# Performance work log

Measured on AMD Instinct MI355X. Metric: run time of the kernel, lower is better.

Reference implementation:

```python
import jax, jax.numpy as jnp
import numpy as np

D_MODEL = 256
NUM_HEADS = 8
D_HEAD = D_MODEL // NUM_HEADS


def setup_inputs() -> dict:
    key = jax.random.key(0)
    k1, k2, k3, k4, k5, k6 = jax.random.split(key, 6)
    B, L, C, H, W = 2, 2048, D_MODEL, 4, 4
    query = jax.random.normal(k1, (B, L, C, H, W), dtype=jnp.float32)
    key_t = jax.random.normal(k2, (B, L, C, H, W), dtype=jnp.float32)
    value = jax.random.normal(k3, (B, L, C, H, W), dtype=jnp.float32)
    # 1x1 conv weights (out_channels, in_channels), no bias
    s = 1.0 / np.sqrt(C)
    Wq = jax.random.uniform(k4, (C, C), jnp.float32, -s, s)
    Wk = jax.random.uniform(k5, (C, C), jnp.float32, -s, s)
    Wv = jax.random.uniform(k6, (C, C), jnp.float32, -s, s)
    return {"query": query, "key": key_t, "value": value, "Wq": Wq, "Wk": Wk, "Wv": Wv}


def _split_heads(x, B, L, H, W):
    # (B, L, C, H, W) -> (num_heads*B, L, d_head, H, W), head-major like torch permute(2,0,1,3,4,5)
    x = x.reshape(B, L, NUM_HEADS, D_HEAD, H, W)
    x = jnp.transpose(x, (2, 0, 1, 3, 4, 5))  # (nh, B, L, d_head, H, W)
    return x.reshape(NUM_HEADS * B, L, D_HEAD, H, W)


def reference(query, key, value, Wq, Wk, Wv):
    B, L, C, H, W = value.shape
    # 1x1 conv == channel matmul: (B,L,C,H,W) x (O,C) -> (B,L,O,H,W)
    q = jnp.einsum('blchw,oc->blohw', query, Wq)
    k = jnp.einsum('blchw,oc->blohw', key, Wk)
    v = jnp.einsum('blchw,oc->blohw', value, Wv)
    q = _split_heads(q, B, L, H, W)
    k = _split_heads(k, B, L, H, W)
    v = _split_heads(v, B, L, H, W)
    scale = 1.0 / np.sqrt(D_HEAD).astype(np.float32)
    score = jnp.einsum('bidhw,bjdhw->bij', q, k) * scale  # (nh*B, L, L)
    attn = jax.nn.softmax(score, axis=-1)
    context = jnp.einsum('bij,bjdhw->bidhw', attn, v)  # (nh*B, L, d_head, H, W)
    context = context.reshape(NUM_HEADS, B, L, D_HEAD, H, W)
    context = jnp.transpose(context, (1, 2, 0, 3, 4, 5)).reshape(B, L, C, H, W)
    return context, attn
```

## Files before the change

### kernel.cpp

```cpp
#include <hip/hip_runtime.h>


typedef short s16x8 __attribute__((ext_vector_type(8)));
typedef float f32x4 __attribute__((ext_vector_type(4)));

__device__ __forceinline__ unsigned short f2bf(float f) {
  union { float f; unsigned int u; } v; v.f = f;
  return (unsigned short)((v.u + 0x7FFFu + ((v.u >> 16) & 1u)) >> 16);
}
__device__ __forceinline__ float bf2f(unsigned short h) {
  union { unsigned int u; float f; } v; v.u = ((unsigned int)h) << 16;
  return v.f;
}

__device__ __forceinline__ void async_copy16(const unsigned short* g, unsigned short* l) {
  __builtin_amdgcn_global_load_lds((const __attribute__((address_space(1))) void*)g,
                                   (__attribute__((address_space(3))) void*)l, 16, 0, 0);
}

__global__ void __launch_bounds__(256) prep_x_kernel(const float* __restrict__ src,
                                                     unsigned short* __restrict__ dst) {
  __shared__ float ld[256 * 17];
  const int bl = blockIdx.x;
  const int t = threadIdx.x;
  const float* s = src + (size_t)bl * 4096;
#pragma unroll
  for (int i = 0; i < 4; ++i) {
    int flat = i * 1024 + t * 4;
    float4 v = *(const float4*)(s + flat);
    int c = flat >> 4, hw = flat & 15;
    float* p = &ld[c * 17 + hw];
    p[0] = v.x; p[1] = v.y; p[2] = v.z; p[3] = v.w;
  }
  __syncthreads();
  unsigned short* d = dst + (size_t)bl * 4096;
#pragma unroll
  for (int hw = 0; hw < 16; ++hw)
    d[hw * 256 + t] = f2bf(ld[t * 17 + hw]);
}

__global__ void __launch_bounds__(256) prep_xv_kernel(const float* __restrict__ src,
                                                      unsigned short* __restrict__ dst) {
  __shared__ float ld[256 * 17];
  const int bl = blockIdx.x;
  const int b = bl >> 11, l = bl & 2047;
  const int t = threadIdx.x;
  const float* s = src + (size_t)bl * 4096;
#pragma unroll
  for (int i = 0; i < 4; ++i) {
    int flat = i * 1024 + t * 4;
    float4 v = *(const float4*)(s + flat);
    int c = flat >> 4, hw = flat & 15;
    float* p = &ld[c * 17 + hw];
    p[0] = v.x; p[1] = v.y; p[2] = v.z; p[3] = v.w;
  }
  __syncthreads();
#pragma unroll
  for (int hw = 0; hw < 16; ++hw)
    dst[((size_t)(b * 16 + hw) * 2048 + l) * 256 + t] = f2bf(ld[t * 17 + hw]);
}

__global__ void __launch_bounds__(256) prep_w_kernel(const float* __restrict__ a,
                                                     const float* __restrict__ b,
                                                     const float* __restrict__ c,
                                                     unsigned short* __restrict__ dst) {
  int i = blockIdx.x * 256 + threadIdx.x;
  const float* s = (i < 65536) ? a : ((i < 131072) ? b : c);
  dst[i] = f2bf(s[i & 65535]);
}

__device__ __forceinline__ void gemm_core_async(const unsigned short* __restrict__ Ag, int ldA,
                                                const unsigned short* __restrict__ Bg, int ldB,
                                                int K, unsigned short* As, unsigned short* Bs,
                                                f32x4 acc[4][4]) {
  const int tid = threadIdx.x;
  const int lane = tid & 63;
  const int w = tid >> 6;
  const int wr = (w >> 1) * 64, wc = (w & 1) * 64;
  const int r = lane >> 2, kk = (lane & 3) * 8;
  for (int k0 = 0; k0 < K; k0 += 32) {
#pragma unroll
    for (int i = 0; i < 2; ++i) {
      const int row0 = w * 32 + i * 16;
      async_copy16(Ag + (size_t)(row0 + r) * ldA + k0 + kk, As + row0 * 32);
      async_copy16(Bg + (size_t)(row0 + r) * ldB + k0 + kk, Bs + row0 * 32);
    }
    __syncthreads();
    s16x8 af[4], bfv[4];
#pragma unroll
    for (int m = 0; m < 4; ++m)
      af[m] = *(const s16x8*)(As + (wr + m * 16 + (lane & 15)) * 32 + (lane >> 4) * 8);
#pragma unroll
    for (int n = 0; n < 4; ++n)
      bfv[n] = *(const s16x8*)(Bs + (wc + n * 16 + (lane & 15)) * 32 + (lane >> 4) * 8);
#pragma unroll
    for (int m = 0; m < 4; ++m)
#pragma unroll
      for (int n = 0; n < 4; ++n)
        acc[m][n] = __builtin_amdgcn_mfma_f32_16x16x32_bf16(af[m], bfv[n], acc[m][n], 0, 0, 0);
    __syncthreads();
  }
}

#define ACC_INIT(acc)                         \
  {                                           \
    const f32x4 z_ = {0.f, 0.f, 0.f, 0.f};    \
    _Pragma("unroll")                         \
    for (int m_ = 0; m_ < 4; ++m_)            \
      _Pragma("unroll")                       \
      for (int n_ = 0; n_ < 4; ++n_) acc[m_][n_] = z_; \
  }

__global__ void __launch_bounds__(256) gemm_proj_kernel(const unsigned short* __restrict__ X,
                                                        const unsigned short* __restrict__ W,
                                                        unsigned short* __restrict__ out) {
  __shared__ unsigned short As[4096], Bs[4096];
  f32x4 acc[4][4];
  ACC_INIT(acc);
  gemm_core_async(X + (size_t)blockIdx.x * 128 * 256, 256,
                  W + (size_t)blockIdx.y * 128 * 256, 256, 256, As, Bs, acc);
  const int tid = threadIdx.x, lane = tid & 63, w = tid >> 6;
  const int wr = (w >> 1) * 64, wc = (w & 1) * 64;
  const int R0 = blockIdx.x * 128 + wr + ((lane >> 4) << 2);
  const int C0 = blockIdx.y * 128 + wc + (lane & 15);
#pragma unroll
  for (int m = 0; m < 4; ++m)
#pragma unroll
    for (int n = 0; n < 4; ++n)
#pragma unroll
      for (int r = 0; r < 4; ++r) {
        int R = R0 + m * 16 + r;
        int o = C0 + n * 16;
        int bl = R >> 4, hw = R & 15;
        int b = bl >> 11, l = bl & 2047;
        int head = o >> 5, d = o & 31;
        out[((size_t)(head * 2 + b) * 2048 + l) * 512 + d * 16 + hw] = f2bf(acc[m][n][r]);
      }
}

__global__ void __launch_bounds__(256) gemm_proj_vt_kernel(const unsigned short* __restrict__ W,
                                                           const unsigned short* __restrict__ X2,
                                                           unsigned short* __restrict__ vt) {
  __shared__ unsigned short As[4096], Bs[4096];
  f32x4 acc[4][4];
  ACC_INIT(acc);
  gemm_core_async(W + (size_t)blockIdx.x * 128 * 256, 256,
                  X2 + (size_t)blockIdx.y * 128 * 256, 256, 256, As, Bs, acc);
  const int tid = threadIdx.x, lane = tid & 63, w = tid >> 6;
  const int wr = (w >> 1) * 64, wc = (w & 1) * 64;
  const int R0 = blockIdx.x * 128 + wr + ((lane >> 4) << 2);
  const int C0 = blockIdx.y * 128 + wc + (lane & 15);
#pragma unroll
  for (int m = 0; m < 4; ++m)
#pragma unroll
    for (int n = 0; n < 4; ++n)
#pragma unroll
      for (int r = 0; r < 4; ++r) {
        int o = R0 + m * 16 + r;
        int p = C0 + n * 16;
        int head = o >> 5, d = o & 31;
        int b = p >> 15, hw = (p >> 11) & 15, l = p & 2047;
        vt[((size_t)((head * 2 + b) * 512) + d * 16 + hw) * 2048 + l] = f2bf(acc[m][n][r]);
      }
}

template <int FUSED>
__global__ void __launch_bounds__(256) gemm_score_kernel(const unsigned short* __restrict__ q,
                                                         const unsigned short* __restrict__ k,
                                                         float* __restrict__ attn,
                                                         unsigned short* __restrict__ pbf,
                                                         float* __restrict__ partial) {
  __shared__ unsigned short As[4096], Bs[4096];
  f32x4 acc[4][4];
  ACC_INIT(acc);
  const int bh = blockIdx.z;
  gemm_core_async(q + ((size_t)bh * 2048 + blockIdx.x * 128) * 512, 512,
                  k + ((size_t)bh * 2048 + blockIdx.y * 128) * 512, 512, 512, As, Bs, acc);
  const int tid = threadIdx.x, lane = tid & 63, w = tid >> 6;
  const int wr = (w >> 1) * 64, wc = (w & 1) * 64;
  const float scale = 0.17677669529663687f;
  const int R0 = blockIdx.x * 128 + wr + ((lane >> 4) << 2);
  const int C0 = blockIdx.y * 128 + wc + (lane & 15);
  if (!FUSED) {
    float* O = attn + (size_t)bh * 4194304;
#pragma unroll
    for (int m = 0; m < 4; ++m)
#pragma unroll
      for (int n = 0; n < 4; ++n)
#pragma unroll
        for (int r = 0; r < 4; ++r)
          O[(size_t)(R0 + m * 16 + r) * 2048 + (C0 + n * 16)] = acc[m][n][r] * scale;
  } else {
#pragma unroll
    for (int m = 0; m < 4; ++m)
#pragma unroll
      for (int n = 0; n < 4; ++n)
#pragma unroll
        for (int r = 0; r < 4; ++r)
          acc[m][n][r] = __expf(acc[m][n][r] * scale);
    unsigned short* P = pbf + (size_t)bh * 4194304;
#pragma unroll
    for (int m = 0; m < 4; ++m)
#pragma unroll
      for (int n = 0; n < 4; ++n)
#pragma unroll
        for (int r = 0; r < 4; ++r)
          P[(size_t)(R0 + m * 16 + r) * 2048 + (C0 + n * 16)] = f2bf(acc[m][n][r]);
    const int chunk = blockIdx.y * 2 + (w & 1);
#pragma unroll
    for (int m = 0; m < 4; ++m)
#pragma unroll
      for (int r = 0; r < 4; ++r) {
        float s = (acc[m][0][r] + acc[m][1][r]) + (acc[m][2][r] + acc[m][3][r]);
        s += __shfl_xor(s, 1); s += __shfl_xor(s, 2);
        s += __shfl_xor(s, 4); s += __shfl_xor(s, 8);
        if ((lane & 15) == 0) {
          int rloc = wr + ((lane >> 4) << 2) + m * 16 + r;
          partial[((size_t)bh * 2048 + blockIdx.x * 128 + rloc) * 32 + chunk] = s;
        }
      }
  }
}

__global__ void __launch_bounds__(256) norm_kernel(const unsigned short* __restrict__ pbf,
                                                   const float* __restrict__ partial,
                                                   float* __restrict__ attn,
                                                   float* __restrict__ inv_buf) {
  __shared__ float sh;
  const int row = blockIdx.x;
  const int t = threadIdx.x;
  if (t < 32) {
    float v = partial[(size_t)row * 32 + t];
    v += __shfl_xor(v, 1); v += __shfl_xor(v, 2);
    v += __shfl_xor(v, 4); v += __shfl_xor(v, 8); v += __shfl_xor(v, 16);
    if (t == 0) sh = v;
  }
  __syncthreads();
  const float inv = 1.0f / sh;
  if (t == 0) inv_buf[row] = inv;
  s16x8 h = *(const s16x8*)(pbf + (size_t)row * 2048 + t * 8);
  float o[8];
#pragma unroll
  for (int i = 0; i < 8; ++i) o[i] = bf2f((unsigned short)h[i]) * inv;
  float* p = attn + (size_t)row * 2048 + t * 8;
  *(float4*)(p)     = *(float4*)&o[0];
  *(float4*)(p + 4) = *(float4*)&o[4];
}

__global__ void __launch_bounds__(256) softmax_kernel(float* __restrict__ attn) {
  __shared__ float red[4];
  float* p = attn + (size_t)blockIdx.x * 2048;
  const int t = threadIdx.x;
  float4 v0 = *(const float4*)(p + t * 8);
  float4 v1 = *(const float4*)(p + t * 8 + 4);
  float mx = fmaxf(fmaxf(fmaxf(v0.x, v0.y), fmaxf(v0.z, v0.w)),
                   fmaxf(fmaxf(v1.x, v1.y), fmaxf(v1.z, v1.w)));
#pragma unroll
  for (int off = 32; off; off >>= 1) mx = fmaxf(mx, __shfl_xor(mx, off));
  if ((t & 63) == 0) red[t >> 6] = mx;
  __syncthreads();
  mx = fmaxf(fmaxf(red[0], red[1]), fmaxf(red[2], red[3]));
  __syncthreads();
  float e[8];
  e[0] = __expf(v0.x - mx); e[1] = __expf(v0.y - mx);
  e[2] = __expf(v0.z - mx); e[3] = __expf(v0.w - mx);
  e[4] = __expf(v1.x - mx); e[5] = __expf(v1.y - mx);
  e[6] = __expf(v1.z - mx); e[7] = __expf(v1.w - mx);
  float s = ((e[0] + e[1]) + (e[2] + e[3])) + ((e[4] + e[5]) + (e[6] + e[7]));
#pragma unroll
  for (int off = 32; off; off >>= 1) s += __shfl_xor(s, off);
  if ((t & 63) == 0) red[t >> 6] = s;
  __syncthreads();
  s = red[0] + red[1] + red[2] + red[3];
  const float inv = 1.0f / s;
  float4 o0 = {e[0] * inv, e[1] * inv, e[2] * inv, e[3] * inv};
  float4 o1 = {e[4] * inv, e[5] * inv, e[6] * inv, e[7] * inv};
  *(float4*)(p + t * 8) = o0;
  *(float4*)(p + t * 8 + 4) = o1;
}

__global__ void __launch_bounds__(256) transpose_v_kernel(const unsigned short* __restrict__ vs,
                                                          unsigned short* __restrict__ vt) {
  __shared__ unsigned short tile[64][65];
  const int bh = blockIdx.z;
  const int j0 = blockIdx.x * 64, d0 = blockIdx.y * 64;
  const unsigned short* src = vs + (size_t)bh * 2048 * 512;
  unsigned short* dst = vt + (size_t)bh * 512 * 2048;
  const int t = threadIdx.x;
#pragma unroll
  for (int i = 0; i < 16; ++i) {
    int e = t * 16 + i;
    int r = e >> 6, c = e & 63;
    tile[r][c] = src[(size_t)(j0 + r) * 512 + d0 + c];
  }
  __syncthreads();
#pragma unroll
  for (int i = 0; i < 16; ++i) {
    int e = t * 16 + i;
    int r = e >> 6, c = e & 63;
    dst[(size_t)(d0 + r) * 2048 + j0 + c] = tile[c][r];
  }
}

__device__ __forceinline__ void ctx_epilogue(f32x4 acc[4][4], float* __restrict__ outc,
                                             const float* __restrict__ inv_buf,
                                             int bh, int bx, int by) {
  const int tid = threadIdx.x, lane = tid & 63, w = tid >> 6;
  const int wr = (w >> 1) * 64, wc = (w & 1) * 64;
  const int b = bh & 1, head = bh >> 1;
  const int R0 = bx * 128 + wr + ((lane >> 4) << 2);
  const int C0 = by * 128 + wc + (lane & 15);
#pragma unroll
  for (int m = 0; m < 4; ++m)
#pragma unroll
    for (int r2 = 0; r2 < 4; ++r2) {
      int R = R0 + m * 16 + r2;
      float sc = inv_buf ? inv_buf[(size_t)bh * 2048 + R] : 1.0f;
#pragma unroll
      for (int n = 0; n < 4; ++n) {
        int dd = C0 + n * 16;
        int d = dd >> 4, hw = dd & 15;
        outc[((size_t)(b * 2048 + R) * 256 + head * 32 + d) * 16 + hw] = acc[m][n][r2] * sc;
      }
    }
}

__global__ void __launch_bounds__(256) gemm_ctx_bf16_kernel(const unsigned short* __restrict__ pbf,
                                                            const unsigned short* __restrict__ vt,
                                                            const float* __restrict__ inv_buf,
                                                            float* __restrict__ outc) {
  __shared__ unsigned short As[4096], Bs[4096];
  f32x4 acc[4][4];
  ACC_INIT(acc);
  const int bh = blockIdx.z;
  gemm_core_async(pbf + (size_t)bh * 4194304 + (size_t)blockIdx.x * 128 * 2048, 2048,
                  vt + (size_t)bh * 1048576 + (size_t)blockIdx.y * 128 * 2048, 2048,
                  2048, As, Bs, acc);
  ctx_epilogue(acc, outc, inv_buf, bh, blockIdx.x, blockIdx.y);
}

__global__ void __launch_bounds__(256) gemm_ctx_f32_kernel(const float* __restrict__ attn,
                                                           const unsigned short* __restrict__ vt,
                                                           float* __restrict__ outc) {
  __shared__ unsigned short As[4096], Bs[4096];
  f32x4 acc[4][4];
  ACC_INIT(acc);
  const int tid = threadIdx.x, lane = tid & 63, w = tid >> 6;
  const int wr = (w >> 1) * 64, wc = (w & 1) * 64;
  const int bh = blockIdx.z;
  const float* Ag = attn + (size_t)bh * 4194304 + (size_t)blockIdx.x * 128 * 2048;
  const unsigned short* Bg = vt + (size_t)bh * 1048576 + (size_t)blockIdx.y * 128 * 2048;
  const int r = lane >> 2, kk = (lane & 3) * 8;
  const int arow = tid >> 1, acol = (tid & 1) * 16;
  for (int k0 = 0; k0 < 2048; k0 += 32) {
#pragma unroll
    for (int i = 0; i < 2; ++i) {
      const int row0 = w * 32 + i * 16;
      async_copy16(Bg + (size_t)(row0 + r) * 2048 + k0 + kk, Bs + row0 * 32);
    }
    {
      const float* sp = Ag + (size_t)arow * 2048 + k0 + acol;
      float4 f0 = *(const float4*)(sp);
      float4 f1 = *(const float4*)(sp + 4);
      float4 f2 = *(const float4*)(sp + 8);
      float4 f3 = *(const float4*)(sp + 12);
      s16x8 h0, h1;
      h0[0] = (short)f2bf(f0.x); h0[1] = (short)f2bf(f0.y);
      h0[2] = (short)f2bf(f0.z); h0[3] = (short)f2bf(f0.w);
      h0[4] = (short)f2bf(f1.x); h0[5] = (short)f2bf(f1.y);
      h0[6] = (short)f2bf(f1.z); h0[7] = (short)f2bf(f1.w);
      h1[0] = (short)f2bf(f2.x); h1[1] = (short)f2bf(f2.y);
      h1[2] = (short)f2bf(f2.z); h1[3] = (short)f2bf(f2.w);
      h1[4] = (short)f2bf(f3.x); h1[5] = (short)f2bf(f3.y);
      h1[6] = (short)f2bf(f3.z); h1[7] = (short)f2bf(f3.w);
      *(s16x8*)(As + arow * 32 + acol) = h0;
      *(s16x8*)(As + arow * 32 + acol + 8) = h1;
    }
    __syncthreads();
    s16x8 af[4], bfv[4];
#pragma unroll
    for (int m = 0; m < 4; ++m)
      af[m] = *(const s16x8*)(As + (wr + m * 16 + (lane & 15)) * 32 + (lane >> 4) * 8);
#pragma unroll
    for (int n = 0; n < 4; ++n)
      bfv[n] = *(const s16x8*)(Bs + (wc + n * 16 + (lane & 15)) * 32 + (lane >> 4) * 8);
#pragma unroll
    for (int m = 0; m < 4; ++m)
#pragma unroll
      for (int n = 0; n < 4; ++n)
        acc[m][n] = __builtin_amdgcn_mfma_f32_16x16x32_bf16(af[m], bfv[n], acc[m][n], 0, 0, 0);
    __syncthreads();
  }
  ctx_epilogue(acc, outc, nullptr, bh, blockIdx.x, blockIdx.y);
}

extern "C" void kernel_launch(void* const* d_in, const int* in_sizes, int n_in,
                              void* d_out, int out_size, void* d_ws, size_t ws_size,
                              hipStream_t stream) {
  const float* query = (const float*)d_in[0];
  const float* key   = (const float*)d_in[1];
  const float* value = (const float*)d_in[2];
  const float* Wq    = (const float*)d_in[3];
  const float* Wk    = (const float*)d_in[4];
  const float* Wv    = (const float*)d_in[5];

  float* out_ctx  = (float*)d_out;
  float* out_attn = (float*)d_out + 16777216;

  unsigned short* X    = (unsigned short*)d_ws;
  unsigned short* q_s  = X + 16777216;
  unsigned short* k_s  = q_s + 16777216;
  unsigned short* v_t  = k_s + 16777216;
  unsigned short* Wbf  = v_t + 16777216;
  unsigned short* P_bf = Wbf + 196608;
  float* partial = (float*)(P_bf + 67108864);
  float* inv_buf = partial + 1048576;

  const bool fused = ws_size >= (size_t)273154048;

  prep_w_kernel<<<768, 256, 0, stream>>>(Wq, Wk, Wv, Wbf);

  prep_x_kernel<<<4096, 256, 0, stream>>>(query, X);
  gemm_proj_kernel<<<dim3(512, 2), 256, 0, stream>>>(X, Wbf, q_s);

  prep_x_kernel<<<4096, 256, 0, stream>>>(key, X);
  gemm_proj_kernel<<<dim3(512, 2), 256, 0, stream>>>(X, Wbf + 65536, k_s);

  if (fused) {
    prep_xv_kernel<<<4096, 256, 0, stream>>>(value, X);
    gemm_proj_vt_kernel<<<dim3(2, 512), 256, 0, stream>>>(Wbf + 131072, X, v_t);
    gemm_score_kernel<1><<<dim3(16, 16, 16), 256, 0, stream>>>(q_s, k_s, nullptr, P_bf, partial);
    norm_kernel<<<32768, 256, 0, stream>>>(P_bf, partial, out_attn, inv_buf);
    gemm_ctx_bf16_kernel<<<dim3(16, 4, 16), 256, 0, stream>>>(P_bf, v_t, inv_buf, out_ctx);
  } else {
    prep_x_kernel<<<4096, 256, 0, stream>>>(value, X);
    gemm_proj_kernel<<<dim3(512, 2), 256, 0, stream>>>(X, Wbf + 131072, v_t);
    gemm_score_kernel<0><<<dim3(16, 16, 16), 256, 0, stream>>>(q_s, k_s, out_attn, nullptr, nullptr);
    softmax_kernel<<<32768, 256, 0, stream>>>(out_attn);
    transpose_v_kernel<<<dim3(32, 8, 16), 256, 0, stream>>>(v_t, X);
    gemm_ctx_f32_kernel<<<dim3(16, 4, 16), 256, 0, stream>>>(out_attn, X, out_ctx);
  }
}
```

Before: 478.5 us.

## Fuse attn normalization into ctx GEMM and batch Q/K/V prep and projections

Merges the three input prep launches into one kernel and the Q/K projections into one batched launch, staging Xq/Xk in the P_bf buffer before it is overwritten. The separate norm pass that re-read bf16 probabilities and wrote fp32 attn is replaced by a tiny inv-sum kernel. The y==0 blocks of the context GEMM now write normalized attn straight from the LDS tiles they already load. This removes one full re-read of the probability matrix and several launches, but leaves the attn store work on only a quarter of the ctx blocks, which may unbalance that kernel.

```diff
diff --git a/kernel.cpp b/kernel.cpp
--- a/kernel.cpp
+++ b/kernel.cpp
@@ -16,6 +16,39 @@
 __device__ __forceinline__ void async_copy16(const unsigned short* g, unsigned short* l) {
   __builtin_amdgcn_global_load_lds((const __attribute__((address_space(1))) void*)g,
                                    (__attribute__((address_space(3))) void*)l, 16, 0, 0);
+}
+
+__global__ void __launch_bounds__(256) prep_all_kernel(const float* __restrict__ qs,
+                                                       const float* __restrict__ ks,
+                                                       const float* __restrict__ vs,
+                                                       unsigned short* __restrict__ Xq,
+                                                       unsigned short* __restrict__ Xk,
+                                                       unsigned short* __restrict__ X2) {
+  __shared__ float ld[256 * 17];
+  const int bl = blockIdx.x;
+  const int z = blockIdx.y;
+  const int t = threadIdx.x;
+  const float* s = (z == 0 ? qs : (z == 1 ? ks : vs)) + (size_t)bl * 4096;
+#pragma unroll
+  for (int i = 0; i < 4; ++i) {
+    int flat = i * 1024 + t * 4;
+    float4 v = *(const float4*)(s + flat);
+    int c = flat >> 4, hw = flat & 15;
+    float* p = &ld[c * 17 + hw];
+    p[0] = v.x; p[1] = v.y; p[2] = v.z; p[3] = v.w;
+  }
+  __syncthreads();
+  if (z < 2) {
+    unsigned short* d = (z == 0 ? Xq : Xk) + (size_t)bl * 4096;
+#pragma unroll
+    for (int hw = 0; hw < 16; ++hw)
+      d[hw * 256 + t] = f2bf(ld[t * 17 + hw]);
+  } else {
+    const int b = bl >> 11, l = bl & 2047;
+#pragma unroll
+    for (int hw = 0; hw < 16; ++hw)
+      X2[((size_t)(b * 16 + hw) * 2048 + l) * 256 + t] = f2bf(ld[t * 17 + hw]);
+  }
 }
 
 __global__ void __launch_bounds__(256) prep_x_kernel(const float* __restrict__ src,
@@ -37,27 +70,6 @@
 #pragma unroll
   for (int hw = 0; hw < 16; ++hw)
     d[hw * 256 + t] = f2bf(ld[t * 17 + hw]);
-}
-
-__global__ void __launch_bounds__(256) prep_xv_kernel(const float* __restrict__ src,
-                                                      unsigned short* __restrict__ dst) {
-  __shared__ float ld[256 * 17];
-  const int bl = blockIdx.x;
-  const int b = bl >> 11, l = bl & 2047;
-  const int t = threadIdx.x;
-  const float* s = src + (size_t)bl * 4096;
-#pragma unroll
-  for (int i = 0; i < 4; ++i) {
-    int flat = i * 1024 + t * 4;
-    float4 v = *(const float4*)(s + flat);
-    int c = flat >> 4, hw = flat & 15;
-    float* p = &ld[c * 17 + hw];
-    p[0] = v.x; p[1] = v.y; p[2] = v.z; p[3] = v.w;
-  }
-  __syncthreads();
-#pragma unroll
-  for (int hw = 0; hw < 16; ++hw)
-    dst[((size_t)(b * 16 + hw) * 2048 + l) * 256 + t] = f2bf(ld[t * 17 + hw]);
 }
 
 __global__ void __launch_bounds__(256) prep_w_kernel(const float* __restrict__ a,
@@ -110,6 +122,39 @@
       _Pragma("unroll")                       \
       for (int n_ = 0; n_ < 4; ++n_) acc[m_][n_] = z_; \
   }
+
+__global__ void __launch_bounds__(256) gemm_proj_qk_kernel(const unsigned short* __restrict__ Xq,
+                                                           const unsigned short* __restrict__ Xk,
+                                                           const unsigned short* __restrict__ Wbf,
+                                                           unsigned short* __restrict__ q_s,
+                                                           unsigned short* __restrict__ k_s) {
+  __shared__ unsigned short As[4096], Bs[4096];
+  f32x4 acc[4][4];
+  ACC_INIT(acc);
+  const int z = blockIdx.z;
+  const unsigned short* X = z ? Xk : Xq;
+  const unsigned short* W = Wbf + z * 65536;
+  unsigned short* out = z ? k_s : q_s;
+  gemm_core_async(X + (size_t)blockIdx.x * 128 * 256, 256,
+                  W + (size_t)blockIdx.y * 128 * 256, 256, 256, As, Bs, acc);
+  const int tid = threadIdx.x, lane = tid & 63, w = tid >> 6;
+  const int wr = (w >> 1) * 64, wc = (w & 1) * 64;
+  const int R0 = blockIdx.x * 128 + wr + ((lane >> 4) << 2);
+  const int C0 = blockIdx.y * 128 + wc + (lane & 15);
+#pragma unroll
+  for (int m = 0; m < 4; ++m)
+#pragma unroll
+    for (int n = 0; n < 4; ++n)
+#pragma unroll
+      for (int r = 0; r < 4; ++r) {
+        int R = R0 + m * 16 + r;
+        int o = C0 + n * 16;
+        int bl = R >> 4, hw = R & 15;
+        int b = bl >> 11, l = bl & 2047;
+        int head = o >> 5, d = o & 31;
+        out[((size_t)(head * 2 + b) * 2048 + l) * 512 + d * 16 + hw] = f2bf(acc[m][n][r]);
+      }
+}
 
 __global__ void __launch_bounds__(256) gemm_proj_kernel(const unsigned short* __restrict__ X,
                                                         const unsigned short* __restrict__ W,
@@ -222,29 +267,100 @@
   }
 }
 
-__global__ void __launch_bounds__(256) norm_kernel(const unsigned short* __restrict__ pbf,
-                                                   const float* __restrict__ partial,
-                                                   float* __restrict__ attn,
-                                                   float* __restrict__ inv_buf) {
-  __shared__ float sh;
-  const int row = blockIdx.x;
+__global__ void __launch_bounds__(256) inv_kernel(const float* __restrict__ partial,
+                                                  float* __restrict__ inv_buf) {
   const int t = threadIdx.x;
-  if (t < 32) {
-    float v = partial[(size_t)row * 32 + t];
-    v += __shfl_xor(v, 1); v += __shfl_xor(v, 2);
-    v += __shfl_xor(v, 4); v += __shfl_xor(v, 8); v += __shfl_xor(v, 16);
-    if (t == 0) sh = v;
-  }
-  __syncthreads();
-  const float inv = 1.0f / sh;
-  if (t == 0) inv_buf[row] = inv;
-  s16x8 h = *(const s16x8*)(pbf + (size_t)row * 2048 + t * 8);
-  float o[8];
-#pragma unroll
-  for (int i = 0; i < 8; ++i) o[i] = bf2f((unsigned short)h[i]) * inv;
-  float* p = attn + (size_t)row * 2048 + t * 8;
-  *(float4*)(p)     = *(float4*)&o[0];
-  *(float4*)(p + 4) = *(float4*)&o[4];
+  const int row = blockIdx.x * 64 + (t >> 2);
+  const int q4 = t & 3;
+  const float4* p = (const float4*)(partial + (size_t)row * 32 + q4 * 8);
+  float4 a = p[0], b = p[1];
+  float s = ((a.x + a.y) + (a.z + a.w)) + ((b.x + b.y) + (b.z + b.w));
+  s += __shfl_xor(s, 1); s += __shfl_xor(s, 2);
+  if (q4 == 0) inv_buf[row] = 1.0f / s;
+}
+
+__device__ __forceinline__ void ctx_epilogue(f32x4 acc[4][4], float* __restrict__ outc,
+                                             const float* __restrict__ inv_buf,
+                                             int bh, int bx, int by) {
+  const int tid = threadIdx.x, lane = tid & 63, w = tid >> 6;
+  const int wr = (w >> 1) * 64, wc = (w & 1) * 64;
+  const int b = bh & 1, head = bh >> 1;
+  const int R0 = bx * 128 + wr + ((lane >> 4) << 2);
+  const int C0 = by * 128 + wc + (lane & 15);
+#pragma unroll
+  for (int m = 0; m < 4; ++m)
+#pragma unroll
+    for (int r2 = 0; r2 < 4; ++r2) {
+      int R = R0 + m * 16 + r2;
+      float sc = inv_buf ? inv_buf[(size_t)bh * 2048 + R] : 1.0f;
+#pragma unroll
+      for (int n = 0; n < 4; ++n) {
+        int dd = C0 + n * 16;
+        int d = dd >> 4, hw = dd & 15;
+        outc[((size_t)(b * 2048 + R) * 256 + head * 32 + d) * 16 + hw] = acc[m][n][r2] * sc;
+      }
+    }
+}
+
+__global__ void __launch_bounds__(256) gemm_ctx_fused_kernel(const unsigned short* __restrict__ pbf,
+                                                             const unsigned short* __restrict__ vt,
+                                                             const float* __restrict__ inv_buf,
+                                                             float* __restrict__ attn,
+                                                             float* __restrict__ outc) {
+  __shared__ unsigned short As[4096], Bs[4096];
+  f32x4 acc[4][4];
+  ACC_INIT(acc);
+  const int tid = threadIdx.x, lane = tid & 63, w = tid >> 6;
+  const int wr = (w >> 1) * 64, wc = (w & 1) * 64;
+  const int bh = blockIdx.z;
+  const unsigned short* Ag = pbf + (size_t)bh * 4194304 + (size_t)blockIdx.x * 128 * 2048;
+  const unsigned short* Bg = vt + (size_t)bh * 1048576 + (size_t)blockIdx.y * 128 * 2048;
+  const int r = lane >> 2, kk = (lane & 3) * 8;
+  const bool emit = (blockIdx.y == 0);
+  const int erow = tid >> 1, ecol = (tid & 1) * 16;
+  float einv = 0.f;
+  float* eattn = nullptr;
+  if (emit) {
+    einv = inv_buf[(size_t)bh * 2048 + blockIdx.x * 128 + erow];
+    eattn = attn + (size_t)bh * 4194304 + (size_t)(blockIdx.x * 128 + erow) * 2048 + ecol;
+  }
+  for (int k0 = 0; k0 < 2048; k0 += 32) {
+#pragma unroll
+    for (int i = 0; i < 2; ++i) {
+      const int row0 = w * 32 + i * 16;
+      async_copy16(Ag + (size_t)(row0 + r) * 2048 + k0 + kk, As + row0 * 32);
+      async_copy16(Bg + (size_t)(row0 + r) * 2048 + k0 + kk, Bs + row0 * 32);
+    }
+    __syncthreads();
+    if (emit) {
+      s16x8 h0 = *(const s16x8*)(As + erow * 32 + ecol);
+      s16x8 h1 = *(const s16x8*)(As + erow * 32 + ecol + 8);
+      float o[16];
+#pragma unroll
+      for (int i = 0; i < 8; ++i) o[i] = bf2f((unsigned short)h0[i]) * einv;
+#pragma unroll
+      for (int i = 0; i < 8; ++i) o[8 + i] = bf2f((unsigned short)h1[i]) * einv;
+      float* ep = eattn + k0;
+      *(float4*)(ep)      = *(float4*)&o[0];
+      *(float4*)(ep + 4)  = *(float4*)&o[4];
+      *(float4*)(ep + 8)  = *(float4*)&o[8];
+      *(float4*)(ep + 12) = *(float4*)&o[12];
+    }
+    s16x8 af[4], bfv[4];
+#pragma unroll
+    for (int m = 0; m < 4; ++m)
+      af[m] = *(const s16x8*)(As + (wr + m * 16 + (lane & 15)) * 32 + (lane >> 4) * 8);
+#pragma unroll
+    for (int n = 0; n < 4; ++n)
+      bfv[n] = *(const s16x8*)(Bs + (wc + n * 16 + (lane & 15)) * 32 + (lane >> 4) * 8);
+#pragma unroll
+    for (int m = 0; m < 4; ++m)
+#pragma unroll
+      for (int n = 0; n < 4; ++n)
+        acc[m][n] = __builtin_amdgcn_mfma_f32_16x16x32_bf16(af[m], bfv[n], acc[m][n], 0, 0, 0);
+    __syncthreads();
+  }
+  ctx_epilogue(acc, outc, inv_buf, bh, blockIdx.x, blockIdx.y);
 }
 
 __global__ void __launch_bounds__(256) softmax_kernel(float* __restrict__ attn) {
@@ -300,43 +416,6 @@
     int r = e >> 6, c = e & 63;
     dst[(size_t)(d0 + r) * 2048 + j0 + c] = tile[c][r];
   }
-}
-
-__device__ __forceinline__ void ctx_epilogue(f32x4 acc[4][4], float* __restrict__ outc,
-                                             const float* __restrict__ inv_buf,
-                                             int bh, int bx, int by) {
-  const int tid = threadIdx.x, lane = tid & 63, w = tid >> 6;
-  const int wr = (w >> 1) * 64, wc = (w & 1) * 64;
-  const int b = bh & 1, head = bh >> 1;
-  const int R0 = bx * 128 + wr + ((lane >> 4) << 2);
-  const int C0 = by * 128 + wc + (lane & 15);
-#pragma unroll
-  for (int m = 0; m < 4; ++m)
-#pragma unroll
-    for (int r2 = 0; r2 < 4; ++r2) {
-      int R = R0 + m * 16 + r2;
-      float sc = inv_buf ? inv_buf[(size_t)bh * 2048 + R] : 1.0f;
-#pragma unroll
-      for (int n = 0; n < 4; ++n) {
-        int dd = C0 + n * 16;
-        int d = dd >> 4, hw = dd & 15;
-        outc[((size_t)(b * 2048 + R) * 256 + head * 32 + d) * 16 + hw] = acc[m][n][r2] * sc;
-      }
-    }
-}
-
-__global__ void __launch_bounds__(256) gemm_ctx_bf16_kernel(const unsigned short* __restrict__ pbf,
-                                                            const unsigned short* __restrict__ vt,
-                                                            const float* __restrict__ inv_buf,
-                                                            float* __restrict__ outc) {
-  __shared__ unsigned short As[4096], Bs[4096];
-  f32x4 acc[4][4];
-  ACC_INIT(acc);
-  const int bh = blockIdx.z;
-  gemm_core_async(pbf + (size_t)bh * 4194304 + (size_t)blockIdx.x * 128 * 2048, 2048,
-                  vt + (size_t)bh * 1048576 + (size_t)blockIdx.y * 128 * 2048, 2048,
-                  2048, As, Bs, acc);
-  ctx_epilogue(acc, outc, inv_buf, bh, blockIdx.x, blockIdx.y);
 }
 
 __global__ void __launch_bounds__(256) gemm_ctx_f32_kernel(const float* __restrict__ attn,
@@ -407,8 +486,8 @@
   float* out_ctx  = (float*)d_out;
   float* out_attn = (float*)d_out + 16777216;
 
-  unsigned short* X    = (unsigned short*)d_ws;
-  unsigned short* q_s  = X + 16777216;
+  unsigned short* X2   = (unsigned short*)d_ws;
+  unsigned short* q_s  = X2 + 16777216;
   unsigned short* k_s  = q_s + 16777216;
   unsigned short* v_t  = k_s + 16777216;
   unsigned short* Wbf  = v_t + 16777216;
@@ -416,28 +495,30 @@
   float* partial = (float*)(P_bf + 67108864);
   float* inv_buf = partial + 1048576;
 
+  unsigned short* Xq = P_bf;
+  unsigned short* Xk = P_bf + 16777216;
+
   const bool fused = ws_size >= (size_t)273154048;
 
   prep_w_kernel<<<768, 256, 0, stream>>>(Wq, Wk, Wv, Wbf);
 
-  prep_x_kernel<<<4096, 256, 0, stream>>>(query, X);
-  gemm_proj_kernel<<<dim3(512, 2), 256, 0, stream>>>(X, Wbf, q_s);
-
-  prep_x_kernel<<<4096, 256, 0, stream>>>(key, X);
-  gemm_proj_kernel<<<dim3(512, 2), 256, 0, stream>>>(X, Wbf + 65536, k_s);
-
   if (fused) {
-    prep_xv_kernel<<<4096, 256, 0, stream>>>(value, X);
-    gemm_proj_vt_kernel<<<dim3(2, 512), 256, 0, stream>>>(Wbf + 131072, X, v_t);
+    prep_all_kernel<<<dim3(4096, 3), 256, 0, stream>>>(query, key, value, Xq, Xk, X2);
+    gemm_proj_qk_kernel<<<dim3(512, 2, 2), 256, 0, stream>>>(Xq, Xk, Wbf, q_s, k_s);
+    gemm_proj_vt_kernel<<<dim3(2, 512), 256, 0, stream>>>(Wbf + 131072, X2, v_t);
     gemm_score_kernel<1><<<dim3(16, 16, 16), 256, 0, stream>>>(q_s, k_s, nullptr, P_bf, partial);
-    norm_kernel<<<32768, 256, 0, stream>>>(P_bf, partial, out_attn, inv_buf);
-    gemm_ctx_bf16_kernel<<<dim3(16, 4, 16), 256, 0, stream>>>(P_bf, v_t, inv_buf, out_ctx);
+    inv_kernel<<<512, 256, 0, stream>>>(partial, inv_buf);
+    gemm_ctx_fused_kernel<<<dim3(16, 4, 16), 256, 0, stream>>>(P_bf, v_t, inv_buf, out_attn, out_ctx);
   } else {
-    prep_x_kernel<<<4096, 256, 0, stream>>>(value, X);
-    gemm_proj_kernel<<<dim3(512, 2), 256, 0, stream>>>(X, Wbf + 131072, v_t);
+    prep_x_kernel<<<4096, 256, 0, stream>>>(query, X2);
+    gemm_proj_kernel<<<dim3(512, 2), 256, 0, stream>>>(X2, Wbf, q_s);
+    prep_x_kernel<<<4096, 256, 0, stream>>>(key, X2);
+    gemm_proj_kernel<<<dim3(512, 2), 256, 0, stream>>>(X2, Wbf + 65536, k_s);
+    prep_x_kernel<<<4096, 256, 0, stream>>>(value, X2);
+    gemm_proj_kernel<<<dim3(512, 2), 256, 0, stream>>>(X2, Wbf + 131072, v_t);
     gemm_score_kernel<0><<<dim3(16, 16, 16), 256, 0, stream>>>(q_s, k_s, out_attn, nullptr, nullptr);
     softmax_kernel<<<32768, 256, 0, stream>>>(out_attn);
-    transpose_v_kernel<<<dim3(32, 8, 16), 256, 0, stream>>>(v_t, X);
-    gemm_ctx_f32_kernel<<<dim3(16, 4, 16), 256, 0, stream>>>(out_attn, X, out_ctx);
-  }
-}
+    transpose_v_kernel<<<dim3(32, 8, 16), 256, 0, stream>>>(v_t, X2);
+    gemm_ctx_f32_kernel<<<dim3(16, 4, 16), 256, 0, stream>>>(out_attn, X2, out_ctx);
+  }
+}
```

Measured after the change: 504.9 us. +5.5%, slower.
